# Performance work log

Hardware: AMD Instinct MI355X
Metric: run time of the kernel (lower is better)

Reference implementation:

```python
import jax, jax.numpy as jnp
import numpy as np

HEAD_SIZE = 64
NUM_HEADS = 16
D_MODEL = HEAD_SIZE * NUM_HEADS  # 1024
B, S = 2, 2048


def setup_inputs() -> dict:
    key = jax.random.key(0)
    ks = jax.random.split(key, 13)
    sc = 1.0 / np.sqrt(D_MODEL)
    inp = {
        'queries': jax.random.normal(ks[0], (B, S, D_MODEL), jnp.float32),
        'keys': jax.random.normal(ks[1], (B, S, D_MODEL), jnp.float32),
        'values': jax.random.normal(ks[2], (B, S, D_MODEL), jnp.float32),
        'mask': jax.random.randint(ks[3], (B, NUM_HEADS, S, S), 0, 2, jnp.int32),
        # nn.Linear weights (out,in) and biases
        'Wq': jax.random.normal(ks[4], (D_MODEL, D_MODEL), jnp.float32) * sc,
        'bq': jax.random.normal(ks[5], (D_MODEL,), jnp.float32) * sc,
        'Wk': jax.random.normal(ks[6], (D_MODEL, D_MODEL), jnp.float32) * sc,
        'bk': jax.random.normal(ks[7], (D_MODEL,), jnp.float32) * sc,
        'Wv': jax.random.normal(ks[8], (D_MODEL, D_MODEL), jnp.float32) * sc,
        'bv': jax.random.normal(ks[9], (D_MODEL,), jnp.float32) * sc,
        'Wy': jax.random.normal(ks[10], (D_MODEL, D_MODEL), jnp.float32) * sc,
        'by': jax.random.normal(ks[11], (D_MODEL,), jnp.float32) * sc,
        # extra nn.Parameter biases (initialized to zeros in the module)
        'bq2': jnp.zeros((D_MODEL,), jnp.float32),
        'bk2': jnp.zeros((D_MODEL,), jnp.float32),
        'bv2': jnp.zeros((D_MODEL,), jnp.float32),
        'by2': jnp.zeros((D_MODEL,), jnp.float32),
    }
    return inp


def _split_heads(x):
    b, s, _ = x.shape
    return x.reshape(b, s, NUM_HEADS, HEAD_SIZE).transpose(0, 2, 1, 3)  # [B,H,S,D]


def _merge_heads(x):
    b, h, s, d = x.shape
    return x.transpose(0, 2, 1, 3).reshape(b, s, h * d)


def mha(queries, keys, values, mask, Wq, bq, bq2, Wk, bk, bk2, Wv, bv, bv2, Wy, by, by2):
    q = queries @ Wq.T + bq + bq2
    k = keys @ Wk.T + bk + bk2
    v = values @ Wv.T + bv + bv2
    q, k, v = _split_heads(q), _split_heads(k), _split_heads(v)  # [B,H,S,D]
    scores = jnp.einsum('bhqd,bhkd->bhqk', q, k) / np.sqrt(HEAD_SIZE).astype(np.float32)
    m = mask.astype(scores.dtype)
    scores = scores * m - 1e4 * (1.0 - m)
    w = jax.nn.softmax(scores, axis=-1)
    out = jnp.einsum('bhqk,bhkd->bhqd', w, v)
    y = _merge_heads(out)  # [B,S,H*D]
    return y @ Wy.T + by + by2


def reference(queries, keys, values, mask, Wq, bq, Wk, bk, Wv, bv, Wy, by, bq2, bk2, bv2, by2):
    return mha(queries, keys, values, mask, Wq, bq, bq2, Wk, bk, bk2, Wv, bv, bv2, Wy, by, by2)
```

## Files before the change

kernel.cpp:

```cpp
#include <hip/hip_runtime.h>
#include <math.h>


typedef _Float16 h8 __attribute__((ext_vector_type(8)));
typedef _Float16 h4 __attribute__((ext_vector_type(4)));
typedef float f4 __attribute__((ext_vector_type(4)));

#define S_LEN 2048
#define DM 1024
#define NH 16
#define HD 64

__global__ __launch_bounds__(256, 2) void qkv_proj_kernel(
    const float* __restrict__ Xq, const float* __restrict__ Xk, const float* __restrict__ Xv,
    const float* __restrict__ Wq, const float* __restrict__ Wk, const float* __restrict__ Wv,
    const float* __restrict__ bq, const float* __restrict__ bk, const float* __restrict__ bv,
    const float* __restrict__ bq2, const float* __restrict__ bk2, const float* __restrict__ bv2,
    _Float16* __restrict__ oq, _Float16* __restrict__ okk, _Float16* __restrict__ ov)
{
    const int z = blockIdx.z;
    const float* X  = (z == 0) ? Xq  : (z == 1) ? Xk  : Xv;
    const float* W  = (z == 0) ? Wq  : (z == 1) ? Wk  : Wv;
    const float* b1 = (z == 0) ? bq  : (z == 1) ? bk  : bv;
    const float* b2 = (z == 0) ? bq2 : (z == 1) ? bk2 : bv2;
    _Float16* outp  = (z == 0) ? oq  : (z == 1) ? okk : ov;

    __shared__ _Float16 As[128][72];
    __shared__ _Float16 Bs[128][72];

    const int tid  = threadIdx.x;
    const int lane = tid & 63;
    const int wave = tid >> 6;
    const int l16  = lane & 15;
    const int g    = lane >> 4;
    const int wm   = (wave >> 1) * 64;
    const int wn   = (wave & 1) * 64;
    const int m0   = blockIdx.x * 128;
    const int n0   = blockIdx.y * 128;

    f4 acc[4][4] = {};

    for (int k0 = 0; k0 < 1024; k0 += 64) {
        __syncthreads();
        #pragma unroll
        for (int r = 0; r < 8; ++r) {
            int u = tid + 256 * r;
            int row = u >> 4;
            int c4  = (u & 15) * 4;
            f4 xa = *(const f4*)(X + (size_t)(m0 + row) * 1024 + k0 + c4);
            f4 xb = *(const f4*)(W + (size_t)(n0 + row) * 1024 + k0 + c4);
            h4 ha = { (_Float16)xa.x, (_Float16)xa.y, (_Float16)xa.z, (_Float16)xa.w };
            h4 hb = { (_Float16)xb.x, (_Float16)xb.y, (_Float16)xb.z, (_Float16)xb.w };
            *(h4*)&As[row][c4] = ha;
            *(h4*)&Bs[row][c4] = hb;
        }
        __syncthreads();

        #pragma unroll
        for (int ks = 0; ks < 2; ++ks) {
            h8 af[4], bf[4];
            #pragma unroll
            for (int i = 0; i < 4; ++i) af[i] = *(const h8*)&As[wm + i * 16 + l16][ks * 32 + g * 8];
            #pragma unroll
            for (int j = 0; j < 4; ++j) bf[j] = *(const h8*)&Bs[wn + j * 16 + l16][ks * 32 + g * 8];
            #pragma unroll
            for (int i = 0; i < 4; ++i)
                #pragma unroll
                for (int j = 0; j < 4; ++j)
                    acc[i][j] = __builtin_amdgcn_mfma_f32_16x16x32_f16(af[i], bf[j], acc[i][j], 0, 0, 0);
        }
    }

    #pragma unroll
    for (int i = 0; i < 4; ++i)
        #pragma unroll
        for (int j = 0; j < 4; ++j)
            #pragma unroll
            for (int r = 0; r < 4; ++r) {
                int gm = m0 + wm + i * 16 + g * 4 + r;
                int gn = n0 + wn + j * 16 + l16;
                float val = acc[i][j][r] + b1[gn] + b2[gn];
                int b = gm >> 11, s = gm & 2047;
                int h = gn >> 6,  d = gn & 63;
                outp[(((size_t)(b * NH + h) * S_LEN + s) << 6) + d] = (_Float16)val;
            }
}

__global__ __launch_bounds__(256) void transpose_v_kernel(
    const _Float16* __restrict__ v, _Float16* __restrict__ vt)
{
    const int bh = blockIdx.x;
    const int s0 = blockIdx.y * 64;
    __shared__ _Float16 t[64][65];
    const int tid = threadIdx.x;

    #pragma unroll
    for (int r = 0; r < 2; ++r) {
        int u = tid + 256 * r;
        int row = u >> 3, c8 = (u & 7) * 8;
        h8 hv = *(const h8*)(v + ((size_t)bh * S_LEN + s0 + row) * 64 + c8);
        #pragma unroll
        for (int e = 0; e < 8; ++e) t[row][c8 + e] = hv[e];
    }
    __syncthreads();
    #pragma unroll
    for (int r = 0; r < 2; ++r) {
        int u = tid + 256 * r;
        int d = u >> 3, p8 = (u & 7) * 8;
        h8 hv;
        #pragma unroll
        for (int e = 0; e < 8; ++e) {
            int p = p8 + e;
            int c = (p & 3) * 16 + (p >> 2);
            hv[e] = t[c][d];
        }
        *(h8*)(vt + ((size_t)bh * 64 + d) * S_LEN + s0 + p8) = hv;
    }
}

__global__ __launch_bounds__(256, 2) void attn_kernel(
    const _Float16* __restrict__ q_ws, const _Float16* __restrict__ k_ws,
    const _Float16* __restrict__ vt_ws, const int* __restrict__ mask,
    _Float16* __restrict__ o_ws)
{
    const int tid  = threadIdx.x;
    const int lane = tid & 63;
    const int wave = tid >> 6;
    const int g    = lane >> 4;
    const int l16  = lane & 15;
    const int qt   = blockIdx.x;
    const int bh   = blockIdx.y;
    const int q0   = qt * 128;

    __shared__ _Float16 Ks[2][64][72];
    __shared__ _Float16 Vs[2][64][72];
    __shared__ _Float16 Ps[128][72];
    __shared__ unsigned int Ms[2][4][128];

    h8 qf[2][2];
    #pragma unroll
    for (int i = 0; i < 2; ++i)
        #pragma unroll
        for (int ks = 0; ks < 2; ++ks)
            qf[i][ks] = *(const h8*)(q_ws +
                ((size_t)bh * S_LEN + q0 + wave * 32 + i * 16 + l16) * 64 + ks * 32 + g * 8);

    f4 oacc[2][4] = {};
    float lsum[2][4] = {};

    const _Float16* kbase = k_ws + (size_t)bh * S_LEN * 64;
    const _Float16* vbase = vt_ws + (size_t)bh * 64 * S_LEN;
    const int* mbase = mask + ((size_t)bh * S_LEN + q0 + wave * 32) * S_LEN;

    const int srow = tid >> 3;
    const int sc8  = (tid & 7) * 8;

    {
        h8 k0r[2], v0r[2];
        #pragma unroll
        for (int r = 0; r < 2; ++r) {
            int row = srow + 32 * r;
            k0r[r] = *(const h8*)(kbase + (size_t)row * 64 + sc8);
            v0r[r] = *(const h8*)(vbase + (size_t)row * S_LEN + sc8);
        }
        int4 m0r[8];
        #pragma unroll
        for (int c = 0; c < 8; ++c) {
            int chunk = 64 * c + lane;
            m0r[c] = *(const int4*)(mbase + (size_t)(chunk >> 4) * S_LEN + (chunk & 15) * 4);
        }
        #pragma unroll
        for (int r = 0; r < 2; ++r) {
            int row = srow + 32 * r;
            *(h8*)&Ks[0][row][sc8] = k0r[r];
            *(h8*)&Vs[0][row][sc8] = v0r[r];
        }
        #pragma unroll
        for (int c = 0; c < 8; ++c) {
            int chunk = 64 * c + lane;
            unsigned nib = (unsigned)(m0r[c].x != 0)
                         | ((unsigned)(m0r[c].y != 0) << 1)
                         | ((unsigned)(m0r[c].z != 0) << 2)
                         | ((unsigned)(m0r[c].w != 0) << 3);
            int rr = chunk >> 4, c4 = chunk & 15;
            ((unsigned char*)&Ms[0][wave][0])[rr * 16 + (c4 & 3) * 4 + (c4 >> 2)] =
                (unsigned char)nib;
        }
    }
    __syncthreads();

    for (int kt = 0; kt < 32; ++kt) {
        const int cur = kt & 1;
        const int nxt = cur ^ 1;

        h8 knr[2], vnr[2];
        int4 mnr[8];
        if (kt < 31) {
            const int k1 = (kt + 1) * 64;
            #pragma unroll
            for (int r = 0; r < 2; ++r) {
                int row = srow + 32 * r;
                knr[r] = *(const h8*)(kbase + (size_t)(k1 + row) * 64 + sc8);
                vnr[r] = *(const h8*)(vbase + (size_t)row * S_LEN + k1 + sc8);
            }
            #pragma unroll
            for (int c = 0; c < 8; ++c) {
                int chunk = 64 * c + lane;
                mnr[c] = *(const int4*)(mbase + (size_t)(chunk >> 4) * S_LEN + k1 + (chunk & 15) * 4);
            }
        }

        f4 sacc[2][4] = {};
        #pragma unroll
        for (int ks = 0; ks < 2; ++ks) {
            h8 kf[4];
            #pragma unroll
            for (int j = 0; j < 4; ++j) kf[j] = *(const h8*)&Ks[cur][j * 16 + l16][ks * 32 + g * 8];
            #pragma unroll
            for (int i = 0; i < 2; ++i)
                #pragma unroll
                for (int j = 0; j < 4; ++j)
                    sacc[i][j] = __builtin_amdgcn_mfma_f32_16x16x32_f16(qf[i][ks], kf[j], sacc[i][j], 0, 0, 0);
        }

        #pragma unroll
        for (int i = 0; i < 2; ++i)
            #pragma unroll
            for (int r = 0; r < 4; ++r) {
                int row_local = i * 16 + g * 4 + r;
                unsigned word = Ms[cur][wave][row_local * 4 + (l16 >> 2)];
                unsigned sh = l16 & 3;
                float p0 = ((word >> (sh))      & 1u) ? __expf(fmaf(sacc[i][0][r], 0.125f, -5.0f)) : 0.0f;
                float p1 = ((word >> (8 + sh))  & 1u) ? __expf(fmaf(sacc[i][1][r], 0.125f, -5.0f)) : 0.0f;
                float p2 = ((word >> (16 + sh)) & 1u) ? __expf(fmaf(sacc[i][2][r], 0.125f, -5.0f)) : 0.0f;
                float p3 = ((word >> (24 + sh)) & 1u) ? __expf(fmaf(sacc[i][3][r], 0.125f, -5.0f)) : 0.0f;
                lsum[i][r] += (p0 + p1) + (p2 + p3);
                h4 ph = { (_Float16)p0, (_Float16)p1, (_Float16)p2, (_Float16)p3 };
                *(h4*)&Ps[wave * 32 + i * 16 + g * 4 + r][l16 * 4] = ph;
            }

        #pragma unroll
        for (int ks = 0; ks < 2; ++ks) {
            h8 pf[2], vf[4];
            #pragma unroll
            for (int i = 0; i < 2; ++i)  pf[i]  = *(const h8*)&Ps[wave * 32 + i * 16 + l16][ks * 32 + g * 8];
            #pragma unroll
            for (int jd = 0; jd < 4; ++jd) vf[jd] = *(const h8*)&Vs[cur][jd * 16 + l16][ks * 32 + g * 8];
            #pragma unroll
            for (int i = 0; i < 2; ++i)
                #pragma unroll
                for (int jd = 0; jd < 4; ++jd)
                    oacc[i][jd] = __builtin_amdgcn_mfma_f32_16x16x32_f16(pf[i], vf[jd], oacc[i][jd], 0, 0, 0);
        }

        if (kt < 31) {
            #pragma unroll
            for (int r = 0; r < 2; ++r) {
                int row = srow + 32 * r;
                *(h8*)&Ks[nxt][row][sc8] = knr[r];
                *(h8*)&Vs[nxt][row][sc8] = vnr[r];
            }
            #pragma unroll
            for (int c = 0; c < 8; ++c) {
                int chunk = 64 * c + lane;
                unsigned nib = (unsigned)(mnr[c].x != 0)
                             | ((unsigned)(mnr[c].y != 0) << 1)
                             | ((unsigned)(mnr[c].z != 0) << 2)
                             | ((unsigned)(mnr[c].w != 0) << 3);
                int rr = chunk >> 4, c4 = chunk & 15;
                ((unsigned char*)&Ms[nxt][wave][0])[rr * 16 + (c4 & 3) * 4 + (c4 >> 2)] =
                    (unsigned char)nib;
            }
        }
        __syncthreads();
    }

    const int b = bh >> 4, h = bh & 15;
    #pragma unroll
    for (int i = 0; i < 2; ++i)
        #pragma unroll
        for (int r = 0; r < 4; ++r) {
            float l = lsum[i][r];
            l += __shfl_xor(l, 1);
            l += __shfl_xor(l, 2);
            l += __shfl_xor(l, 4);
            l += __shfl_xor(l, 8);
            float inv = 1.0f / l;
            int row = q0 + wave * 32 + i * 16 + g * 4 + r;
            #pragma unroll
            for (int jd = 0; jd < 4; ++jd) {
                int d = jd * 16 + l16;
                o_ws[((size_t)b * S_LEN + row) * DM + h * 64 + d] = (_Float16)(oacc[i][jd][r] * inv);
            }
        }
}

__global__ __launch_bounds__(256, 2) void out_proj_kernel(
    const _Float16* __restrict__ A, const float* __restrict__ W,
    const float* __restrict__ b1, const float* __restrict__ b2,
    float* __restrict__ out)
{
    __shared__ _Float16 As[128][56];
    __shared__ _Float16 Bs[128][56];

    const int tid  = threadIdx.x;
    const int lane = tid & 63;
    const int wave = tid >> 6;
    const int l16  = lane & 15;
    const int g    = lane >> 4;
    const int wm   = (wave >> 1) * 64;
    const int wn   = (wave & 1) * 64;
    const int m0   = blockIdx.x * 128;
    const int n0   = blockIdx.y * 128;

    f4 acc[4][4] = {};

    for (int k0 = 0; k0 < 1024; k0 += 32) {
        __syncthreads();
        #pragma unroll
        for (int r = 0; r < 2; ++r) {
            int u = tid + 256 * r;
            int row = u >> 2, c8 = (u & 3) * 8;
            *(h8*)&As[row][c8] = *(const h8*)(A + (size_t)(m0 + row) * 1024 + k0 + c8);
        }
        #pragma unroll
        for (int r = 0; r < 4; ++r) {
            int f = tid + 256 * r;
            int row = f >> 3, c4 = (f & 7) * 4;
            f4 xb = *(const f4*)(W + (size_t)(n0 + row) * 1024 + k0 + c4);
            h4 hb = { (_Float16)xb.x, (_Float16)xb.y, (_Float16)xb.z, (_Float16)xb.w };
            *(h4*)&Bs[row][c4] = hb;
        }
        __syncthreads();

        h8 af[4], bf[4];
        #pragma unroll
        for (int i = 0; i < 4; ++i) af[i] = *(const h8*)&As[wm + i * 16 + l16][g * 8];
        #pragma unroll
        for (int j = 0; j < 4; ++j) bf[j] = *(const h8*)&Bs[wn + j * 16 + l16][g * 8];
        #pragma unroll
        for (int i = 0; i < 4; ++i)
            #pragma unroll
            for (int j = 0; j < 4; ++j)
                acc[i][j] = __builtin_amdgcn_mfma_f32_16x16x32_f16(af[i], bf[j], acc[i][j], 0, 0, 0);
    }

    #pragma unroll
    for (int i = 0; i < 4; ++i)
        #pragma unroll
        for (int j = 0; j < 4; ++j)
            #pragma unroll
            for (int r = 0; r < 4; ++r) {
                int gm = m0 + wm + i * 16 + g * 4 + r;
                int gn = n0 + wn + j * 16 + l16;
                out[(size_t)gm * 1024 + gn] = acc[i][j][r] + b1[gn] + b2[gn];
            }
}

extern "C" void kernel_launch(void* const* d_in, const int* in_sizes, int n_in,
                              void* d_out, int out_size, void* d_ws, size_t ws_size,
                              hipStream_t stream)
{
    (void)in_sizes; (void)n_in; (void)out_size; (void)ws_size;
    const float* queries = (const float*)d_in[0];
    const float* keys    = (const float*)d_in[1];
    const float* values  = (const float*)d_in[2];
    const int*   mask    = (const int*)d_in[3];
    const float* Wq  = (const float*)d_in[4];
    const float* bq  = (const float*)d_in[5];
    const float* Wk  = (const float*)d_in[6];
    const float* bk  = (const float*)d_in[7];
    const float* Wv  = (const float*)d_in[8];
    const float* bv  = (const float*)d_in[9];
    const float* Wy  = (const float*)d_in[10];
    const float* by  = (const float*)d_in[11];
    const float* bq2 = (const float*)d_in[12];
    const float* bk2 = (const float*)d_in[13];
    const float* bv2 = (const float*)d_in[14];
    const float* by2 = (const float*)d_in[15];
    float* out = (float*)d_out;

    char* ws = (char*)d_ws;
    const size_t MB8 = (size_t)8 * 1024 * 1024;
    _Float16* q_ws  = (_Float16*)(ws);
    _Float16* k_ws  = (_Float16*)(ws + 1 * MB8);
    _Float16* v_ws  = (_Float16*)(ws + 2 * MB8);
    _Float16* vt_ws = (_Float16*)(ws + 3 * MB8);
    _Float16* o_ws  = (_Float16*)(ws + 4 * MB8);

    qkv_proj_kernel<<<dim3(32, 8, 3), 256, 0, stream>>>(
        queries, keys, values, Wq, Wk, Wv, bq, bk, bv, bq2, bk2, bv2,
        q_ws, k_ws, v_ws);
    transpose_v_kernel<<<dim3(32, 32), 256, 0, stream>>>(v_ws, vt_ws);
    attn_kernel<<<dim3(16, 32), 256, 0, stream>>>(q_ws, k_ws, vt_ws, mask, o_ws);
    out_proj_kernel<<<dim3(32, 8), 256, 0, stream>>>(o_ws, Wy, by, by2, out);
}
```

Before: 928.6 us.

## Double-buffer QKV projection tiles with register prefetch of next K slice

The QKV projection GEMM now keeps two shared-memory buffers with a K-step of 32. The next slice is prefetched from global memory into registers while MFMAs run on the current buffer, then converted to fp16 and stored into the other buffer. This drops one barrier per iteration and aims to overlap global load latency with compute. The costs are more live registers per thread and twice as many, smaller k-steps.

```diff
diff --git a/kernel.cpp b/kernel.cpp
--- a/kernel.cpp
+++ b/kernel.cpp
@@ -25,8 +25,8 @@
     const float* b2 = (z == 0) ? bq2 : (z == 1) ? bk2 : bv2;
     _Float16* outp  = (z == 0) ? oq  : (z == 1) ? okk : ov;
 
-    __shared__ _Float16 As[128][72];
-    __shared__ _Float16 Bs[128][72];
+    __shared__ _Float16 As[2][128][56];
+    __shared__ _Float16 Bs[2][128][56];
 
     const int tid  = threadIdx.x;
     const int lane = tid & 63;
@@ -38,37 +38,64 @@
     const int m0   = blockIdx.x * 128;
     const int n0   = blockIdx.y * 128;
 
+    const int urow = tid >> 3;
+    const int uc4  = (tid & 7) * 4;
+
     f4 acc[4][4] = {};
-
-    for (int k0 = 0; k0 < 1024; k0 += 64) {
+    f4 xa[4], xb[4];
+
+    #pragma unroll
+    for (int r = 0; r < 4; ++r) {
+        int row = urow + 32 * r;
+        xa[r] = *(const f4*)(X + (size_t)(m0 + row) * 1024 + uc4);
+        xb[r] = *(const f4*)(W + (size_t)(n0 + row) * 1024 + uc4);
+    }
+    #pragma unroll
+    for (int r = 0; r < 4; ++r) {
+        int row = urow + 32 * r;
+        h4 ha = { (_Float16)xa[r].x, (_Float16)xa[r].y, (_Float16)xa[r].z, (_Float16)xa[r].w };
+        h4 hb = { (_Float16)xb[r].x, (_Float16)xb[r].y, (_Float16)xb[r].z, (_Float16)xb[r].w };
+        *(h4*)&As[0][row][uc4] = ha;
+        *(h4*)&Bs[0][row][uc4] = hb;
+    }
+    __syncthreads();
+
+    for (int ki = 0; ki < 32; ++ki) {
+        const int cur = ki & 1;
+        const int nxt = cur ^ 1;
+
+        if (ki < 31) {
+            const int k1 = (ki + 1) * 32;
+            #pragma unroll
+            for (int r = 0; r < 4; ++r) {
+                int row = urow + 32 * r;
+                xa[r] = *(const f4*)(X + (size_t)(m0 + row) * 1024 + k1 + uc4);
+                xb[r] = *(const f4*)(W + (size_t)(n0 + row) * 1024 + k1 + uc4);
+            }
+        }
+
+        h8 af[4], bf[4];
+        #pragma unroll
+        for (int i = 0; i < 4; ++i) af[i] = *(const h8*)&As[cur][wm + i * 16 + l16][g * 8];
+        #pragma unroll
+        for (int j = 0; j < 4; ++j) bf[j] = *(const h8*)&Bs[cur][wn + j * 16 + l16][g * 8];
+        #pragma unroll
+        for (int i = 0; i < 4; ++i)
+            #pragma unroll
+            for (int j = 0; j < 4; ++j)
+                acc[i][j] = __builtin_amdgcn_mfma_f32_16x16x32_f16(af[i], bf[j], acc[i][j], 0, 0, 0);
+
+        if (ki < 31) {
+            #pragma unroll
+            for (int r = 0; r < 4; ++r) {
+                int row = urow + 32 * r;
+                h4 ha = { (_Float16)xa[r].x, (_Float16)xa[r].y, (_Float16)xa[r].z, (_Float16)xa[r].w };
+                h4 hb = { (_Float16)xb[r].x, (_Float16)xb[r].y, (_Float16)xb[r].z, (_Float16)xb[r].w };
+                *(h4*)&As[nxt][row][uc4] = ha;
+                *(h4*)&Bs[nxt][row][uc4] = hb;
+            }
+        }
         __syncthreads();
-        #pragma unroll
-        for (int r = 0; r < 8; ++r) {
-            int u = tid + 256 * r;
-            int row = u >> 4;
-            int c4  = (u & 15) * 4;
-            f4 xa = *(const f4*)(X + (size_t)(m0 + row) * 1024 + k0 + c4);
-            f4 xb = *(const f4*)(W + (size_t)(n0 + row) * 1024 + k0 + c4);
-            h4 ha = { (_Float16)xa.x, (_Float16)xa.y, (_Float16)xa.z, (_Float16)xa.w };
-            h4 hb = { (_Float16)xb.x, (_Float16)xb.y, (_Float16)xb.z, (_Float16)xb.w };
-            *(h4*)&As[row][c4] = ha;
-            *(h4*)&Bs[row][c4] = hb;
-        }
-        __syncthreads();
-
-        #pragma unroll
-        for (int ks = 0; ks < 2; ++ks) {
-            h8 af[4], bf[4];
-            #pragma unroll
-            for (int i = 0; i < 4; ++i) af[i] = *(const h8*)&As[wm + i * 16 + l16][ks * 32 + g * 8];
-            #pragma unroll
-            for (int j = 0; j < 4; ++j) bf[j] = *(const h8*)&Bs[wn + j * 16 + l16][ks * 32 + g * 8];
-            #pragma unroll
-            for (int i = 0; i < 4; ++i)
-                #pragma unroll
-                for (int j = 0; j < 4; ++j)
-                    acc[i][j] = __builtin_amdgcn_mfma_f32_16x16x32_f16(af[i], bf[j], acc[i][j], 0, 0, 0);
-        }
     }
 
     #pragma unroll
```

After: 913.4 us. Within noise of the previous version (-1.6%).
